# Performance work log

Measured on AMD Instinct MI355X. Metric: run time of the kernel, lower is better.

## Reference

```python
import jax, jax.numpy as jnp
import numpy as np

EMBED_DIM = 1024
NUM_HEAD = 16
HEAD_DIM = EMBED_DIM // NUM_HEAD


def _linear_params(key, in_dim, out_dim):
    kw, kb = jax.random.split(key)
    bound = 1.0 / np.sqrt(in_dim)
    W = jax.random.uniform(kw, (out_dim, in_dim), minval=-bound, maxval=bound, dtype=jnp.float32)
    b = jax.random.uniform(kb, (out_dim,), minval=-bound, maxval=bound, dtype=jnp.float32)
    return W, b


def setup_inputs() -> dict:
    key = jax.random.key(0)
    ks = jax.random.split(key, 7)
    N, S, E = 2, 2048, EMBED_DIM
    k = jax.random.normal(ks[0], (N, S, E), dtype=jnp.float32)
    q = jax.random.normal(ks[1], (N, S, E), dtype=jnp.float32)
    v = jax.random.normal(ks[2], (N, S, E), dtype=jnp.float32)
    Wk, bk = _linear_params(ks[3], E, E)
    Wq, bq = _linear_params(ks[4], E, E)
    Wv, bv = _linear_params(ks[5], E, E)
    Wo, bo = _linear_params(ks[6], E, E)
    return {"key": k, "query": q, "value": v,
            "Wk": Wk, "bk": bk, "Wq": Wq, "bq": bq,
            "Wv": Wv, "bv": bv, "Wo": Wo, "bo": bo}


def reference(key, query, value, Wk, bk, Wq, bq, Wv, bv, Wo, bo):
    N, S_in, E = key.shape
    S_out = query.shape[1]
    H, D = NUM_HEAD, HEAD_DIM
    # projections (torch Linear: x @ W.T + b), split heads -> [N, H, S, D]
    k = (key @ Wk.T + bk).reshape(N, S_in, H, D).transpose(0, 2, 1, 3)
    q = (query @ Wq.T + bq).reshape(N, S_out, H, D).transpose(0, 2, 1, 3)
    v = (value @ Wv.T + bv).reshape(N, S_in, H, D).transpose(0, 2, 1, 3)
    # unfused attention: full [N,H,S_out,S_in] score matrix, scale, softmax
    weight = jnp.einsum("nhqd,nhkd->nhqk", q, k) / jnp.sqrt(jnp.float32(D))
    weight = jax.nn.softmax(weight, axis=-1)
    attn = jnp.einsum("nhqk,nhkd->nhqd", weight, v)  # [N,H,S_out,D]
    attn = attn.transpose(0, 2, 1, 3).reshape(N, S_out, E)
    return attn @ Wo.T + bo
```

## Files before the change

kernel.cpp:

```cpp
#include <hip/hip_runtime.h>

constexpr int E  = 1024;
constexpr int NH = 16;
constexpr int HD = 64;
constexpr int S  = 2048;
constexpr int NB = 2;
constexpr int M  = NB * S;

typedef unsigned short u16;
typedef _Float16 f16;
typedef __attribute__((ext_vector_type(8))) _Float16 h8v;
typedef __attribute__((ext_vector_type(2))) __fp16 hp2v;
typedef __attribute__((ext_vector_type(4))) float f4v;

__device__ __forceinline__ f4v mfmaH(h8v a, h8v b, f4v c) {
    return __builtin_amdgcn_mfma_f32_16x16x32_f16(a, b, c, 0, 0, 0);
}
__device__ __forceinline__ u16 f16bits(float x) {
    union { f16 h; u16 u; } t; t.h = (f16)x; return t.u;
}
__device__ __forceinline__ unsigned pkrtz(float a, float b) {
    union { hp2v h; unsigned u; } t;
    t.h = __builtin_amdgcn_cvt_pkrtz(a, b);
    return t.u;
}
__device__ __forceinline__ float fexp2(float x) {
    float r;
    asm("v_exp_f32 %0, %1" : "=v"(r) : "v"(x));
    return r;
}
typedef const __attribute__((address_space(1))) void gvoid;
typedef __attribute__((address_space(3))) void lvoid;
__device__ __forceinline__ void load_lds16(const u16* g, u16* l) {
    __builtin_amdgcn_global_load_lds((gvoid*)g, (lvoid*)l, 16, 0, 0);
}

__global__ __launch_bounds__(256)
void cvt_f16(const float* __restrict__ wq, const float* __restrict__ wk,
             const float* __restrict__ wv, const float* __restrict__ wo,
             u16* __restrict__ out)
{
    const size_t EE = (size_t)E * E;
    const int z = blockIdx.y;
    const float* src = (z == 0) ? wq : (z == 1) ? wk : (z == 2) ? wv : wo;
    u16* dst = out + (size_t)z * EE;
    for (size_t i = ((size_t)blockIdx.x * 256 + threadIdx.x) * 8; i < EE;
         i += (size_t)gridDim.x * 256 * 8) {
        float4 a = *reinterpret_cast<const float4*>(src + i);
        float4 b = *reinterpret_cast<const float4*>(src + i + 4);
        h8v o;
        o[0] = (f16)a.x; o[1] = (f16)a.y; o[2] = (f16)a.z; o[3] = (f16)a.w;
        o[4] = (f16)b.x; o[5] = (f16)b.y; o[6] = (f16)b.z; o[7] = (f16)b.w;
        *reinterpret_cast<h8v*>(dst + i) = o;
    }
}

__device__ __forceinline__ void gemm16_core(const u16* __restrict__ A,
                                            const u16* __restrict__ W,
                                            int bm, int bn, u16* lds, f4v acc[4][4])
{
    const int tid  = threadIdx.x;
    const int lane = tid & 63;
    const int wid  = tid >> 6;
    const int g = lane >> 4, c = lane & 15;
    const int wr = wid >> 1, wc = wid & 1;
    const int lrow = lane >> 3;
    const int lslot = lane & 7;
    const int sslot = lslot ^ lrow;

    for (int k0 = 0; k0 < E; k0 += 64) {
        #pragma unroll
        for (int i = 0; i < 4; ++i) {
            int rbase = wid * 32 + i * 8;
            load_lds16(A + (size_t)(bm + rbase + lrow) * E + k0 + (sslot << 3),
                       &lds[rbase * 64]);
            load_lds16(W + (size_t)(bn + rbase + lrow) * E + k0 + (sslot << 3),
                       &lds[8192 + rbase * 64]);
        }
        __syncthreads();

        h8v a[4][2];
        #pragma unroll
        for (int mf = 0; mf < 4; ++mf) {
            int row = wr * 64 + mf * 16 + c;
            #pragma unroll
            for (int ks = 0; ks < 2; ++ks)
                a[mf][ks] = *reinterpret_cast<h8v*>(
                    &lds[row * 64 + ((((ks << 2) | g) ^ (c & 7)) << 3)]);
        }
        #pragma unroll
        for (int nf = 0; nf < 4; ++nf) {
            int row = wc * 64 + nf * 16 + c;
            #pragma unroll
            for (int ks = 0; ks < 2; ++ks) {
                h8v b = *reinterpret_cast<h8v*>(
                    &lds[8192 + row * 64 + ((((ks << 2) | g) ^ (c & 7)) << 3)]);
                #pragma unroll
                for (int mf = 0; mf < 4; ++mf)
                    acc[mf][nf] = mfmaH(a[mf][ks], b, acc[mf][nf]);
            }
        }
        __syncthreads();
    }
}

__device__ __forceinline__ void gemm16_core_mixed(const float* __restrict__ A,
                                                  const u16* __restrict__ W,
                                                  int bm, int bn, u16* lds,
                                                  f4v acc[4][4])
{
    const int tid  = threadIdx.x;
    const int lane = tid & 63;
    const int wid  = tid >> 6;
    const int g = lane >> 4, c = lane & 15;
    const int wr = wid >> 1, wc = wid & 1;
    const int lrow = lane >> 3;
    const int lslot = lane & 7;
    const int sslot = lslot ^ lrow;
    const int arow = tid >> 3;
    const int agrp = tid & 7;
    const int aswz = (agrp ^ (arow & 7)) << 3;

    float4 af[4][2];

    #define ALOAD(K0)                                                           \
    {                                                                           \
        _Pragma("unroll")                                                       \
        for (int i = 0; i < 4; ++i) {                                           \
            const float* ap = &A[(size_t)(bm + arow + i * 32) * E + (K0) + agrp * 8]; \
            af[i][0] = *reinterpret_cast<const float4*>(ap);                    \
            af[i][1] = *reinterpret_cast<const float4*>(ap + 4);                \
        }                                                                       \
    }
    #define WSTAGE(K0)                                                          \
    {                                                                           \
        _Pragma("unroll")                                                       \
        for (int i = 0; i < 4; ++i) {                                           \
            int rbase = wid * 32 + i * 8;                                       \
            load_lds16(W + (size_t)(bn + rbase + lrow) * E + (K0) + (sslot << 3),\
                       &lds[8192 + rbase * 64]);                                \
        }                                                                       \
    }
    #define AWRITE()                                                            \
    {                                                                           \
        _Pragma("unroll")                                                       \
        for (int i = 0; i < 4; ++i) {                                           \
            uint4 wv;                                                           \
            wv.x = pkrtz(af[i][0].x, af[i][0].y);                               \
            wv.y = pkrtz(af[i][0].z, af[i][0].w);                               \
            wv.z = pkrtz(af[i][1].x, af[i][1].y);                               \
            wv.w = pkrtz(af[i][1].z, af[i][1].w);                               \
            *reinterpret_cast<uint4*>(&lds[(arow + i * 32) * 64 + aswz]) = wv;  \
        }                                                                       \
    }
    #define GCOMPUTE()                                                          \
    {                                                                           \
        h8v a[4][2];                                                            \
        _Pragma("unroll")                                                       \
        for (int mf = 0; mf < 4; ++mf) {                                        \
            int row = wr * 64 + mf * 16 + c;                                    \
            _Pragma("unroll")                                                   \
            for (int ks = 0; ks < 2; ++ks)                                      \
                a[mf][ks] = *reinterpret_cast<h8v*>(                            \
                    &lds[row * 64 + ((((ks << 2) | g) ^ (c & 7)) << 3)]);       \
        }                                                                       \
        _Pragma("unroll")                                                       \
        for (int nf = 0; nf < 4; ++nf) {                                        \
            int row = wc * 64 + nf * 16 + c;                                    \
            _Pragma("unroll")                                                   \
            for (int ks = 0; ks < 2; ++ks) {                                    \
                h8v b = *reinterpret_cast<h8v*>(                                \
                    &lds[8192 + row * 64 + ((((ks << 2) | g) ^ (c & 7)) << 3)]);\
                _Pragma("unroll")                                               \
                for (int mf = 0; mf < 4; ++mf)                                  \
                    acc[mf][nf] = mfmaH(a[mf][ks], b, acc[mf][nf]);             \
            }                                                                   \
        }                                                                       \
    }

    ALOAD(0);
    WSTAGE(0);
    asm volatile("s_waitcnt vmcnt(4)" ::: "memory");
    AWRITE();
    ALOAD(64);
    asm volatile("s_waitcnt lgkmcnt(0)" ::: "memory");
    asm volatile("s_waitcnt vmcnt(8)" ::: "memory");
    __builtin_amdgcn_s_barrier();
    GCOMPUTE();

    for (int k = 1; k < 15; ++k) {
        __builtin_amdgcn_s_barrier();
        WSTAGE(k * 64);
        asm volatile("s_waitcnt vmcnt(4)" ::: "memory");
        AWRITE();
        ALOAD((k + 1) * 64);
        asm volatile("s_waitcnt lgkmcnt(0)" ::: "memory");
        asm volatile("s_waitcnt vmcnt(8)" ::: "memory");
        __builtin_amdgcn_s_barrier();
        GCOMPUTE();
    }

    __builtin_amdgcn_s_barrier();
    WSTAGE(15 * 64);
    asm volatile("s_waitcnt vmcnt(4)" ::: "memory");
    AWRITE();
    asm volatile("s_waitcnt lgkmcnt(0)" ::: "memory");
    asm volatile("s_waitcnt vmcnt(0)" ::: "memory");
    __builtin_amdgcn_s_barrier();
    GCOMPUTE();

    #undef ALOAD
    #undef WSTAGE
    #undef AWRITE
    #undef GCOMPUTE
}

__global__ __launch_bounds__(256, 3)
void qkv_gemm(const float* __restrict__ query, const float* __restrict__ keyin,
              const float* __restrict__ value,
              const u16* __restrict__ wqf, const u16* __restrict__ wkf,
              const u16* __restrict__ wvf,
              const float* __restrict__ bq, const float* __restrict__ bk,
              const float* __restrict__ bv,
              u16* __restrict__ Qattn, u16* __restrict__ KV, float scaleQ)
{
    __shared__ __align__(16) u16 lds[16384];
    const int z = blockIdx.z;
    const float* A = (z == 0) ? query : (z == 1) ? keyin : value;
    const u16* W = (z == 0) ? wqf : (z == 1) ? wkf : wvf;
    const float* bias = (z == 0) ? bq : (z == 1) ? bk : bv;
    const float scl = (z == 0) ? scaleQ : 1.0f;
    const int bm = blockIdx.x * 128, bn = blockIdx.y * 128;

    f4v acc[4][4];
    #pragma unroll
    for (int a = 0; a < 4; ++a)
        #pragma unroll
        for (int b = 0; b < 4; ++b) acc[a][b] = (f4v){0.f, 0.f, 0.f, 0.f};

    gemm16_core_mixed(A, W, bm, bn, lds, acc);

    const int lane = threadIdx.x & 63;
    const int g = lane >> 4, c = lane & 15;
    const int wid = threadIdx.x >> 6;
    const int wr = wid >> 1, wc = wid & 1;
    float bcol[4];
    #pragma unroll
    for (int nf = 0; nf < 4; ++nf) bcol[nf] = bias[bn + wc * 64 + nf * 16 + c];

    #pragma unroll
    for (int mf = 0; mf < 4; ++mf)
        #pragma unroll
        for (int r = 0; r < 4; ++r) {
            int m  = bm + wr * 64 + mf * 16 + g * 4 + r;
            int nb = m >> 11, sp = m & (S - 1);
            #pragma unroll
            for (int nf = 0; nf < 4; ++nf) {
                int ncol = bn + wc * 64 + nf * 16 + c;
                int h = ncol >> 6, d = ncol & 63;
                int bh_ = nb * NH + h;
                u16 hb = f16bits((acc[mf][nf][r] + bcol[nf]) * scl);
                if (z == 0) {
                    Qattn[((size_t)bh_ * S + sp) * HD + d] = hb;
                } else if (z == 1) {
                    int t = sp >> 6, kk = (sp >> 4) & 3, cc = sp & 15;
                    int ds = d >> 5, gg = (d >> 3) & 3, j = d & 7;
                    KV[((size_t)bh_ * 32 + t) * 8192 +
                       ((size_t)((kk * 2 + ds) * 64 + gg * 16 + cc)) * 8 + j] = hb;
                } else {
                    int t = sp >> 6, rem = sp & 63;
                    int s2 = rem >> 5, bb = (rem >> 4) & 1, gg = (rem >> 2) & 3, a2 = rem & 3;
                    int j = 4 * bb + a2;
                    int df = d >> 4, cc = d & 15;
                    KV[((size_t)bh_ * 32 + t) * 8192 + 4096 +
                       ((size_t)((df * 2 + s2) * 64 + gg * 16 + cc)) * 8 + j] = hb;
                }
            }
        }
}

__global__ __launch_bounds__(256, 3)
void out_gemm(const u16* __restrict__ A, const u16* __restrict__ W,
              const float* __restrict__ bias, float* __restrict__ C)
{
    __shared__ __align__(16) u16 lds[16384];
    const int bm = blockIdx.x * 128, bn = blockIdx.y * 128;
    f4v acc[4][4];
    #pragma unroll
    for (int a = 0; a < 4; ++a)
        #pragma unroll
        for (int b = 0; b < 4; ++b) acc[a][b] = (f4v){0.f, 0.f, 0.f, 0.f};

    gemm16_core(A, W, bm, bn, lds, acc);

    const int lane = threadIdx.x & 63;
    const int g = lane >> 4, c = lane & 15;
    const int wid = threadIdx.x >> 6;
    const int wr = wid >> 1, wc = wid & 1;
    float bcol[4];
    #pragma unroll
    for (int nf = 0; nf < 4; ++nf) bcol[nf] = bias[bn + wc * 64 + nf * 16 + c];

    #pragma unroll
    for (int mf = 0; mf < 4; ++mf)
        #pragma unroll
        for (int r = 0; r < 4; ++r) {
            int m = bm + wr * 64 + mf * 16 + g * 4 + r;
            float* crow = &C[(size_t)m * E + bn + wc * 64];
            #pragma unroll
            for (int nf = 0; nf < 4; ++nf)
                crow[nf * 16 + c] = acc[mf][nf][r] + bcol[nf];
        }
}

__global__ __launch_bounds__(128, 2)
void attn_mfma(const u16* __restrict__ Qf, const u16* __restrict__ KV,
               u16* __restrict__ Out)
{
    __shared__ __align__(16) u16 lds[8192];
    const int tid  = threadIdx.x;
    const int lane = tid & 63;
    const int wid  = tid >> 6;
    const int g = lane >> 4, c = lane & 15;
    const int dlin = blockIdx.x;
    const int idx  = dlin >> 3;
    const int bh = (dlin & 7) * 4 + (idx >> 5);
    const int qc = idx & 31;
    const int n = bh >> 4, h = bh & 15;
    const int q0 = qc * 64 + wid * 32;
    const u16* kvb = KV + (size_t)bh * 32 * 8192;
    const f4v zero4 = {0.f, 0.f, 0.f, 0.f};

    h8v Qb[2][2];
    #pragma unroll
    for (int qf = 0; qf < 2; ++qf)
        #pragma unroll
        for (int ds = 0; ds < 2; ++ds)
            Qb[qf][ds] = *reinterpret_cast<const h8v*>(
                &Qf[((size_t)bh * S + q0 + qf * 16 + c) * HD + ds * 32 + g * 8]);

    h8v ones;
    #pragma unroll
    for (int i = 0; i < 8; ++i) ones[i] = (f16)1.0f;

    f4v oacc[2][4];
    #pragma unroll
    for (int qf = 0; qf < 2; ++qf)
        #pragma unroll
        for (int df = 0; df < 4; ++df) oacc[qf][df] = zero4;
    f4v lacc[2] = {zero4, zero4};

    f4v scA[2][4], scB[2][4];
    h8v vrA[4][2], vrB[4][2];

    #define STAGE_K(T, BUFOFF)                                                  \
    {                                                                           \
        const u16* src = kvb + (size_t)(T) * 8192 + wid * 2048 + lane * 8;      \
        u16* dst = &lds[(BUFOFF) + wid * 2048];                                 \
        _Pragma("unroll")                                                       \
        for (int i = 0; i < 4; ++i) load_lds16(src + i * 512, dst + i * 512);   \
    }
    #define VLOAD(T, VR)                                                        \
    {                                                                           \
        _Pragma("unroll")                                                       \
        for (int df = 0; df < 4; ++df)                                          \
            _Pragma("unroll")                                                   \
            for (int s2 = 0; s2 < 2; ++s2)                                      \
                VR[df][s2] = *reinterpret_cast<const h8v*>(                     \
                    &kvb[(size_t)(T) * 8192 + 4096 +                            \
                         ((size_t)((df * 2 + s2) * 64 + lane)) * 8]);           \
    }

    VLOAD(0, vrA);
    STAGE_K(0, 0);
    STAGE_K(1, 4096);

    asm volatile("s_waitcnt vmcnt(4)" ::: "memory");
    __builtin_amdgcn_s_barrier();
    {
        const u16* Bt = &lds[0];
        #pragma unroll
        for (int qf = 0; qf < 2; ++qf)
            #pragma unroll
            for (int kf = 0; kf < 4; ++kf) scA[qf][kf] = zero4;
        __builtin_amdgcn_s_setprio(1);
        #pragma unroll
        for (int kf = 0; kf < 4; ++kf)
            #pragma unroll
            for (int ds = 0; ds < 2; ++ds) {
                h8v kh = *reinterpret_cast<const h8v*>(
                    &Bt[((size_t)((kf * 2 + ds) * 64 + lane)) * 8]);
                #pragma unroll
                for (int qf = 0; qf < 2; ++qf)
                    scA[qf][kf] = mfmaH(kh, Qb[qf][ds], scA[qf][kf]);
            }
        __builtin_amdgcn_s_setprio(0);
        VLOAD(1, vrB);
    }
    __builtin_amdgcn_s_barrier();
    STAGE_K(2, 0);

    #define PHASE(T, BUFOFF, SCP, SCC, VOLD, WAITN)                             \
    asm volatile("s_waitcnt vmcnt(" WAITN ")" ::: "memory");                    \
    __builtin_amdgcn_s_barrier();                                               \
    {                                                                           \
        const u16* Bt = &lds[BUFOFF];                                           \
        _Pragma("unroll")                                                       \
        for (int qf = 0; qf < 2; ++qf)                                          \
            _Pragma("unroll")                                                   \
            for (int kf = 0; kf < 4; ++kf) SCC[qf][kf] = zero4;                 \
        __builtin_amdgcn_s_setprio(1);                                          \
        _Pragma("unroll")                                                       \
        for (int kf = 0; kf < 4; ++kf)                                          \
            _Pragma("unroll")                                                   \
            for (int ds = 0; ds < 2; ++ds) {                                    \
                h8v kh = *reinterpret_cast<const h8v*>(                         \
                    &Bt[((size_t)((kf * 2 + ds) * 64 + lane)) * 8]);            \
                _Pragma("unroll")                                               \
                for (int qf = 0; qf < 2; ++qf)                                  \
                    SCC[qf][kf] = mfmaH(kh, Qb[qf][ds], SCC[qf][kf]);           \
            }                                                                   \
        __builtin_amdgcn_s_setprio(0);                                          \
        h8v pah[2][2];                                                          \
        _Pragma("unroll")                                                       \
        for (int qf = 0; qf < 2; ++qf)                                          \
            _Pragma("unroll")                                                   \
            for (int s2 = 0; s2 < 2; ++s2) {                                    \
                union { h8v v; unsigned u[4]; } th;                             \
                _Pragma("unroll")                                               \
                for (int kfh = 0; kfh < 2; ++kfh) {                             \
                    int kf = 2 * s2 + kfh;                                      \
                    float p0 = fexp2(SCP[qf][kf][0]);                           \
                    float p1 = fexp2(SCP[qf][kf][1]);                           \
                    float p2 = fexp2(SCP[qf][kf][2]);                           \
                    float p3 = fexp2(SCP[qf][kf][3]);                           \
                    th.u[2 * kfh + 0] = pkrtz(p0, p1);                          \
                    th.u[2 * kfh + 1] = pkrtz(p2, p3);                          \
                }                                                               \
                pah[qf][s2] = th.v;                                             \
            }                                                                   \
        __builtin_amdgcn_s_setprio(1);                                          \
        _Pragma("unroll")                                                       \
        for (int qf = 0; qf < 2; ++qf) {                                        \
            lacc[qf] = mfmaH(pah[qf][0], ones, lacc[qf]);                       \
            lacc[qf] = mfmaH(pah[qf][1], ones, lacc[qf]);                       \
        }                                                                       \
        _Pragma("unroll")                                                       \
        for (int df = 0; df < 4; ++df)                                          \
            _Pragma("unroll")                                                   \
            for (int s2 = 0; s2 < 2; ++s2)                                      \
                _Pragma("unroll")                                               \
                for (int qf = 0; qf < 2; ++qf)                                  \
                    oacc[qf][df] = mfmaH(pah[qf][s2], VOLD[df][s2],             \
                                         oacc[qf][df]);                         \
        __builtin_amdgcn_s_setprio(0);                                          \
        if ((T) + 1 < 32) VLOAD((T) + 1, VOLD);                                 \
    }                                                                           \
    __builtin_amdgcn_s_barrier();                                               \
    if ((T) + 2 < 32) STAGE_K((T) + 2, BUFOFF)

    for (int t = 1; t < 31; t += 2) {
        PHASE(t,     4096, scA, scB, vrA, "12");
        PHASE(t + 1, 0,    scB, scA, vrB, "12");
    }
    PHASE(31, 4096, scA, scB, vrA, "8");
    #undef PHASE
    #undef STAGE_K
    #undef VLOAD

    {
        h8v pah[2][2];
        #pragma unroll
        for (int qf = 0; qf < 2; ++qf)
            #pragma unroll
            for (int s2 = 0; s2 < 2; ++s2) {
                union { h8v v; unsigned u[4]; } th;
                #pragma unroll
                for (int kfh = 0; kfh < 2; ++kfh) {
                    int kf = 2 * s2 + kfh;
                    float p0 = fexp2(scB[qf][kf][0]);
                    float p1 = fexp2(scB[qf][kf][1]);
                    float p2 = fexp2(scB[qf][kf][2]);
                    float p3 = fexp2(scB[qf][kf][3]);
                    th.u[2 * kfh + 0] = pkrtz(p0, p1);
                    th.u[2 * kfh + 1] = pkrtz(p2, p3);
                }
                pah[qf][s2] = th.v;
            }
        #pragma unroll
        for (int qf = 0; qf < 2; ++qf) {
            lacc[qf] = mfmaH(pah[qf][0], ones, lacc[qf]);
            lacc[qf] = mfmaH(pah[qf][1], ones, lacc[qf]);
        }
        #pragma unroll
        for (int df = 0; df < 4; ++df)
            #pragma unroll
            for (int s2 = 0; s2 < 2; ++s2)
                #pragma unroll
                for (int qf = 0; qf < 2; ++qf)
                    oacc[qf][df] = mfmaH(pah[qf][s2], vrB[df][s2], oacc[qf][df]);
    }

    #pragma unroll
    for (int qf = 0; qf < 2; ++qf)
        #pragma unroll
        for (int r = 0; r < 4; ++r) {
            float linv = 1.0f / lacc[qf][r];
            int q = q0 + qf * 16 + g * 4 + r;
            size_t ob = ((size_t)n * S + q) * E + h * HD;
            #pragma unroll
            for (int df = 0; df < 4; ++df)
                Out[ob + df * 16 + c] = f16bits(oacc[qf][df][r] * linv);
        }
}

extern "C" void kernel_launch(void* const* d_in, const int* in_sizes, int n_in,
                              void* d_out, int out_size, void* d_ws, size_t ws_size,
                              hipStream_t stream)
{
    const float* key   = (const float*)d_in[0];
    const float* query = (const float*)d_in[1];
    const float* value = (const float*)d_in[2];
    const float* Wk    = (const float*)d_in[3];
    const float* bk    = (const float*)d_in[4];
    const float* Wq    = (const float*)d_in[5];
    const float* bq    = (const float*)d_in[6];
    const float* Wv    = (const float*)d_in[7];
    const float* bv    = (const float*)d_in[8];
    const float* Wo    = (const float*)d_in[9];
    const float* bo    = (const float*)d_in[10];

    const size_t ME = (size_t)M * E, EE = (size_t)E * E;
    u16* ws16  = (u16*)d_ws;
    u16* wqf   = ws16;
    u16* wkf   = wqf + EE;
    u16* wvf   = wkf + EE;
    u16* wof   = wvf + EE;
    u16* Qattn = wof + EE;
    u16* KV    = Qattn + ME;
    u16* AoutH = KV + 2 * ME;

    const float SCALE_Q = 0.125f * 1.44269504088896340736f;

    cvt_f16<<<dim3(512, 4), 256, 0, stream>>>(Wq, Wk, Wv, Wo, ws16);
    qkv_gemm<<<dim3(M / 128, E / 128, 3), 256, 0, stream>>>(
        query, key, value, wqf, wkf, wvf, bq, bk, bv, Qattn, KV, SCALE_Q);
    attn_mfma<<<dim3((S / 64) * NB * NH), 128, 0, stream>>>(Qattn, KV, AoutH);
    out_gemm<<<dim3(M / 128, E / 128), 256, 0, stream>>>(AoutH, wof, bo, (float*)d_out);
}
```

Baseline: 114.6 us.

## Double-buffer weight tile in LDS for QKV projection GEMM

Adds a second LDS buffer for the weight tile so the next K-step's weights are loaded asynchronously while the current step computes. The loop is unrolled by two to alternate buffers, and the explicit vmcnt wait before compute is dropped. The goal is to hide global-to-LDS latency for the weights. In exchange, LDS per block grows from 32 KB to 48 KB, which may reduce occupancy below the launch-bounds target of 3 blocks.

```diff
diff --git a/kernel.cpp b/kernel.cpp
--- a/kernel.cpp
+++ b/kernel.cpp
@@ -132,13 +132,13 @@
             af[i][1] = *reinterpret_cast<const float4*>(ap + 4);                \
         }                                                                       \
     }
-    #define WSTAGE(K0)                                                          \
+    #define WSTAGE(K0, BUF)                                                     \
     {                                                                           \
         _Pragma("unroll")                                                       \
         for (int i = 0; i < 4; ++i) {                                           \
             int rbase = wid * 32 + i * 8;                                       \
             load_lds16(W + (size_t)(bn + rbase + lrow) * E + (K0) + (sslot << 3),\
-                       &lds[8192 + rbase * 64]);                                \
+                       &lds[(BUF) + rbase * 64]);                               \
         }                                                                       \
     }
     #define AWRITE()                                                            \
@@ -153,7 +153,7 @@
             *reinterpret_cast<uint4*>(&lds[(arow + i * 32) * 64 + aswz]) = wv;  \
         }                                                                       \
     }
-    #define GCOMPUTE()                                                          \
+    #define GCOMPUTE(BUF)                                                       \
     {                                                                           \
         h8v a[4][2];                                                            \
         _Pragma("unroll")                                                       \
@@ -170,7 +170,7 @@
             _Pragma("unroll")                                                   \
             for (int ks = 0; ks < 2; ++ks) {                                    \
                 h8v b = *reinterpret_cast<h8v*>(                                \
-                    &lds[8192 + row * 64 + ((((ks << 2) | g) ^ (c & 7)) << 3)]);\
+                    &lds[(BUF) + row * 64 + ((((ks << 2) | g) ^ (c & 7)) << 3)]);\
                 _Pragma("unroll")                                               \
                 for (int mf = 0; mf < 4; ++mf)                                  \
                     acc[mf][nf] = mfmaH(a[mf][ks], b, acc[mf][nf]);             \
@@ -179,36 +179,38 @@
     }
 
     ALOAD(0);
-    WSTAGE(0);
-    asm volatile("s_waitcnt vmcnt(4)" ::: "memory");
+    WSTAGE(0, 8192);
+    asm volatile("s_waitcnt vmcnt(0)" ::: "memory");
     AWRITE();
+    WSTAGE(64, 16384);
     ALOAD(64);
     asm volatile("s_waitcnt lgkmcnt(0)" ::: "memory");
-    asm volatile("s_waitcnt vmcnt(8)" ::: "memory");
     __builtin_amdgcn_s_barrier();
-    GCOMPUTE();
-
-    for (int k = 1; k < 15; ++k) {
-        __builtin_amdgcn_s_barrier();
-        WSTAGE(k * 64);
-        asm volatile("s_waitcnt vmcnt(4)" ::: "memory");
-        AWRITE();
-        ALOAD((k + 1) * 64);
-        asm volatile("s_waitcnt lgkmcnt(0)" ::: "memory");
-        asm volatile("s_waitcnt vmcnt(8)" ::: "memory");
-        __builtin_amdgcn_s_barrier();
-        GCOMPUTE();
+    GCOMPUTE(8192);
+
+    #define MIX_ITER(K, WBUF_NEXT, WBUF_CUR)                                    \
+    __builtin_amdgcn_s_barrier();                                               \
+    WSTAGE(((K) + 1) * 64, WBUF_NEXT);                                          \
+    asm volatile("s_waitcnt vmcnt(4)" ::: "memory");        \
+    AWRITE();                                                                   \
+    ALOAD(((K) + 1) * 64);                                                      \
+    asm volatile("s_waitcnt lgkmcnt(0)" ::: "memory");                          \
+    __builtin_amdgcn_s_barrier();                                               \
+    GCOMPUTE(WBUF_CUR)
+
+    for (int k = 1; k < 15; k += 2) {
+        MIX_ITER(k,     8192,  16384);
+        MIX_ITER(k + 1, 16384, 8192);
     }
 
     __builtin_amdgcn_s_barrier();
-    WSTAGE(15 * 64);
-    asm volatile("s_waitcnt vmcnt(4)" ::: "memory");
+    asm volatile("s_waitcnt vmcnt(0)" ::: "memory");
     AWRITE();
     asm volatile("s_waitcnt lgkmcnt(0)" ::: "memory");
-    asm volatile("s_waitcnt vmcnt(0)" ::: "memory");
     __builtin_amdgcn_s_barrier();
-    GCOMPUTE();
-
+    GCOMPUTE(16384);
+
+    #undef MIX_ITER
     #undef ALOAD
     #undef WSTAGE
     #undef AWRITE
@@ -224,7 +226,7 @@
               const float* __restrict__ bv,
               u16* __restrict__ Qattn, u16* __restrict__ KV, float scaleQ)
 {
-    __shared__ __align__(16) u16 lds[16384];
+    __shared__ __align__(16) u16 lds[24576];
     const int z = blockIdx.z;
     const float* A = (z == 0) ? query : (z == 1) ? keyin : value;
     const u16* W = (z == 0) ? wqf : (z == 1) ? wkf : wvf;
```

Measured after the change: 124.1 us. 8.2% more time.

## Process two KV tiles per attention phase with doubled LDS staging

Applied to the files above, without the earlier changes.

The attention loop now handles a pair of 64-key tiles per phase (16 phases instead of 32). LDS grows to 32 KB so each wave stages a whole K tile and two pair-buffers double-buffer. The software-pipelined score/PV overlap (scores of tile t+1 computed while softmax-PV of tile t runs) is removed in favour of computing scores and PV within the same phase. This halves barriers and waits per key, but adds register pressure (16 score accumulators, 16 V fragments) and loses the cross-tile overlap, which may reduce occupancy or latency hiding.

```diff
diff --git a/kernel.cpp b/kernel.cpp
--- a/kernel.cpp
+++ b/kernel.cpp
@@ -317,7 +317,7 @@
 void attn_mfma(const u16* __restrict__ Qf, const u16* __restrict__ KV,
                u16* __restrict__ Out)
 {
-    __shared__ __align__(16) u16 lds[8192];
+    __shared__ __align__(16) u16 lds[16384];
     const int tid  = threadIdx.x;
     const int lane = tid & 63;
     const int wid  = tid >> 6;
@@ -350,156 +350,108 @@
         for (int df = 0; df < 4; ++df) oacc[qf][df] = zero4;
     f4v lacc[2] = {zero4, zero4};
 
-    f4v scA[2][4], scB[2][4];
-    h8v vrA[4][2], vrB[4][2];
-
-    #define STAGE_K(T, BUFOFF)                                                  \
-    {                                                                           \
-        const u16* src = kvb + (size_t)(T) * 8192 + wid * 2048 + lane * 8;      \
-        u16* dst = &lds[(BUFOFF) + wid * 2048];                                 \
-        _Pragma("unroll")                                                       \
-        for (int i = 0; i < 4; ++i) load_lds16(src + i * 512, dst + i * 512);   \
-    }
-    #define VLOAD(T, VR)                                                        \
+    h8v vh[4][4];
+
+    #define STAGE_K2(P, BUFOFF)                                                 \
+    {                                                                           \
+        const u16* src = kvb + (size_t)(2 * (P) + wid) * 8192 + lane * 8;       \
+        u16* dst = &lds[(BUFOFF) + wid * 4096];                                 \
+        _Pragma("unroll")                                                       \
+        for (int i = 0; i < 8; ++i) load_lds16(src + i * 512, dst + i * 512);   \
+    }
+    #define VLOAD2(P)                                                           \
     {                                                                           \
         _Pragma("unroll")                                                       \
         for (int df = 0; df < 4; ++df)                                          \
             _Pragma("unroll")                                                   \
-            for (int s2 = 0; s2 < 2; ++s2)                                      \
-                VR[df][s2] = *reinterpret_cast<const h8v*>(                     \
-                    &kvb[(size_t)(T) * 8192 + 4096 +                            \
-                         ((size_t)((df * 2 + s2) * 64 + lane)) * 8]);           \
-    }
-
-    VLOAD(0, vrA);
-    STAGE_K(0, 0);
-    STAGE_K(1, 4096);
-
-    asm volatile("s_waitcnt vmcnt(4)" ::: "memory");
-    __builtin_amdgcn_s_barrier();
-    {
-        const u16* Bt = &lds[0];
-        #pragma unroll
-        for (int qf = 0; qf < 2; ++qf)
-            #pragma unroll
-            for (int kf = 0; kf < 4; ++kf) scA[qf][kf] = zero4;
-        __builtin_amdgcn_s_setprio(1);
-        #pragma unroll
-        for (int kf = 0; kf < 4; ++kf)
-            #pragma unroll
-            for (int ds = 0; ds < 2; ++ds) {
-                h8v kh = *reinterpret_cast<const h8v*>(
-                    &Bt[((size_t)((kf * 2 + ds) * 64 + lane)) * 8]);
-                #pragma unroll
-                for (int qf = 0; qf < 2; ++qf)
-                    scA[qf][kf] = mfmaH(kh, Qb[qf][ds], scA[qf][kf]);
-            }
-        __builtin_amdgcn_s_setprio(0);
-        VLOAD(1, vrB);
-    }
-    __builtin_amdgcn_s_barrier();
-    STAGE_K(2, 0);
-
-    #define PHASE(T, BUFOFF, SCP, SCC, VOLD, WAITN)                             \
+            for (int s2 = 0; s2 < 4; ++s2)                                      \
+                vh[df][s2] = *reinterpret_cast<const h8v*>(                     \
+                    &kvb[(size_t)(2 * (P) + (s2 >> 1)) * 8192 + 4096 +          \
+                         ((size_t)((df * 2 + (s2 & 1)) * 64 + lane)) * 8]);     \
+    }
+
+    #define PHASE2(P, BUFOFF, WAITN)                                            \
     asm volatile("s_waitcnt vmcnt(" WAITN ")" ::: "memory");                    \
     __builtin_amdgcn_s_barrier();                                               \
     {                                                                           \
         const u16* Bt = &lds[BUFOFF];                                           \
+        f4v sc[2][8];                                                           \
         _Pragma("unroll")                                                       \
         for (int qf = 0; qf < 2; ++qf)                                          \
             _Pragma("unroll")                                                   \
-            for (int kf = 0; kf < 4; ++kf) SCC[qf][kf] = zero4;                 \
+            for (int kf = 0; kf < 8; ++kf) sc[qf][kf] = zero4;                  \
         __builtin_amdgcn_s_setprio(1);                                          \
         _Pragma("unroll")                                                       \
-        for (int kf = 0; kf < 4; ++kf)                                          \
+        for (int kf = 0; kf < 8; ++kf) {                                        \
+            int st = kf >> 2, lkf = kf & 3;                                     \
             _Pragma("unroll")                                                   \
             for (int ds = 0; ds < 2; ++ds) {                                    \
                 h8v kh = *reinterpret_cast<const h8v*>(                         \
-                    &Bt[((size_t)((kf * 2 + ds) * 64 + lane)) * 8]);            \
+                    &Bt[st * 4096 +                                             \
+                        ((size_t)((lkf * 2 + ds) * 64 + lane)) * 8]);           \
                 _Pragma("unroll")                                               \
                 for (int qf = 0; qf < 2; ++qf)                                  \
-                    SCC[qf][kf] = mfmaH(kh, Qb[qf][ds], SCC[qf][kf]);           \
+                    sc[qf][kf] = mfmaH(kh, Qb[qf][ds], sc[qf][kf]);             \
             }                                                                   \
+        }                                                                       \
         __builtin_amdgcn_s_setprio(0);                                          \
-        h8v pah[2][2];                                                          \
-        _Pragma("unroll")                                                       \
-        for (int qf = 0; qf < 2; ++qf)                                          \
-            _Pragma("unroll")                                                   \
-            for (int s2 = 0; s2 < 2; ++s2) {                                    \
-                union { h8v v; unsigned u[4]; } th;                             \
+        _Pragma("unroll")                                                       \
+        for (int half = 0; half < 2; ++half) {                                  \
+            h8v pah[2][2];                                                      \
+            _Pragma("unroll")                                                   \
+            for (int qf = 0; qf < 2; ++qf)                                      \
                 _Pragma("unroll")                                               \
-                for (int kfh = 0; kfh < 2; ++kfh) {                             \
-                    int kf = 2 * s2 + kfh;                                      \
-                    float p0 = fexp2(SCP[qf][kf][0]);                           \
-                    float p1 = fexp2(SCP[qf][kf][1]);                           \
-                    float p2 = fexp2(SCP[qf][kf][2]);                           \
-                    float p3 = fexp2(SCP[qf][kf][3]);                           \
-                    th.u[2 * kfh + 0] = pkrtz(p0, p1);                          \
-                    th.u[2 * kfh + 1] = pkrtz(p2, p3);                          \
+                for (int s2l = 0; s2l < 2; ++s2l) {                             \
+                    int s2 = half * 2 + s2l;                                    \
+                    union { h8v v; unsigned u[4]; } th;                         \
+                    _Pragma("unroll")                                           \
+                    for (int kfh = 0; kfh < 2; ++kfh) {                         \
+                        int kf = 2 * s2 + kfh;                                  \
+                        float p0 = fexp2(sc[qf][kf][0]);                        \
+                        float p1 = fexp2(sc[qf][kf][1]);                        \
+                        float p2 = fexp2(sc[qf][kf][2]);                        \
+                        float p3 = fexp2(sc[qf][kf][3]);                        \
+                        th.u[2 * kfh + 0] = pkrtz(p0, p1);                      \
+                        th.u[2 * kfh + 1] = pkrtz(p2, p3);                      \
+                    }                                                           \
+                    pah[qf][s2l] = th.v;                                        \
                 }                                                               \
-                pah[qf][s2] = th.v;                                             \
+            __builtin_amdgcn_s_setprio(1);                                      \
+            _Pragma("unroll")                                                   \
+            for (int qf = 0; qf < 2; ++qf) {                                    \
+                lacc[qf] = mfmaH(pah[qf][0], ones, lacc[qf]);                   \
+                lacc[qf] = mfmaH(pah[qf][1], ones, lacc[qf]);                   \
             }                                                                   \
-        __builtin_amdgcn_s_setprio(1);                                          \
-        _Pragma("unroll")                                                       \
-        for (int qf = 0; qf < 2; ++qf) {                                        \
-            lacc[qf] = mfmaH(pah[qf][0], ones, lacc[qf]);                       \
-            lacc[qf] = mfmaH(pah[qf][1], ones, lacc[qf]);                       \
-        }                                                                       \
-        _Pragma("unroll")                                                       \
-        for (int df = 0; df < 4; ++df)                                          \
-            _Pragma("unroll")                                                   \
-            for (int s2 = 0; s2 < 2; ++s2)                                      \
+            _Pragma("unroll")                                                   \
+            for (int df = 0; df < 4; ++df)                                      \
                 _Pragma("unroll")                                               \
-                for (int qf = 0; qf < 2; ++qf)                                  \
-                    oacc[qf][df] = mfmaH(pah[qf][s2], VOLD[df][s2],             \
-                                         oacc[qf][df]);                         \
-        __builtin_amdgcn_s_setprio(0);                                          \
-        if ((T) + 1 < 32) VLOAD((T) + 1, VOLD);                                 \
+                for (int s2l = 0; s2l < 2; ++s2l)                               \
+                    _Pragma("unroll")                                           \
+                    for (int qf = 0; qf < 2; ++qf)                              \
+                        oacc[qf][df] = mfmaH(pah[qf][s2l],                      \
+                                             vh[df][half * 2 + s2l],            \
+                                             oacc[qf][df]);                     \
+            __builtin_amdgcn_s_setprio(0);                                      \
+        }                                                                       \
+        if ((P) + 1 < 16) VLOAD2((P) + 1);                                      \
     }                                                                           \
     __builtin_amdgcn_s_barrier();                                               \
-    if ((T) + 2 < 32) STAGE_K((T) + 2, BUFOFF)
-
-    for (int t = 1; t < 31; t += 2) {
-        PHASE(t,     4096, scA, scB, vrA, "12");
-        PHASE(t + 1, 0,    scB, scA, vrB, "12");
-    }
-    PHASE(31, 4096, scA, scB, vrA, "8");
-    #undef PHASE
-    #undef STAGE_K
-    #undef VLOAD
-
-    {
-        h8v pah[2][2];
-        #pragma unroll
-        for (int qf = 0; qf < 2; ++qf)
-            #pragma unroll
-            for (int s2 = 0; s2 < 2; ++s2) {
-                union { h8v v; unsigned u[4]; } th;
-                #pragma unroll
-                for (int kfh = 0; kfh < 2; ++kfh) {
-                    int kf = 2 * s2 + kfh;
-                    float p0 = fexp2(scB[qf][kf][0]);
-                    float p1 = fexp2(scB[qf][kf][1]);
-                    float p2 = fexp2(scB[qf][kf][2]);
-                    float p3 = fexp2(scB[qf][kf][3]);
-                    th.u[2 * kfh + 0] = pkrtz(p0, p1);
-                    th.u[2 * kfh + 1] = pkrtz(p2, p3);
-                }
-                pah[qf][s2] = th.v;
-            }
-        #pragma unroll
-        for (int qf = 0; qf < 2; ++qf) {
-            lacc[qf] = mfmaH(pah[qf][0], ones, lacc[qf]);
-            lacc[qf] = mfmaH(pah[qf][1], ones, lacc[qf]);
-        }
-        #pragma unroll
-        for (int df = 0; df < 4; ++df)
-            #pragma unroll
-            for (int s2 = 0; s2 < 2; ++s2)
-                #pragma unroll
-                for (int qf = 0; qf < 2; ++qf)
-                    oacc[qf][df] = mfmaH(pah[qf][s2], vrB[df][s2], oacc[qf][df]);
-    }
+    if ((P) + 2 < 16) STAGE_K2((P) + 2, BUFOFF)
+
+    VLOAD2(0);
+    STAGE_K2(0, 0);
+    STAGE_K2(1, 8192);
+
+    PHASE2(0, 0, "8");
+    for (int p = 1; p < 15; p += 2) {
+        PHASE2(p,     8192, "24");
+        PHASE2(p + 1, 0,    "24");
+    }
+    PHASE2(15, 8192, "16");
+
+    #undef PHASE2
+    #undef STAGE_K2
+    #undef VLOAD2
 
     #pragma unroll
     for (int qf = 0; qf < 2; ++qf)
```

Measured after the change: 115.4 us. About the same (+0.7%).
